# Optimization experiments

Measured on AMD Instinct MI355X. Metric: run time of the kernel, lower is better.

## Reference

```python
import jax, jax.numpy as jnp
import numpy as np

N = 50000      # nodes
E = 800000     # edges (before self-loops)
IN = 256       # input_dim
H = 8          # heads (hard-coded in module)
C = 32         # hidden_dim per head
OUT = 64       # output_dim
NEG_SLOPE = 0.2  # PyG GATConv default leaky_relu slope


def setup_inputs() -> dict:
    key = jax.random.key(0)
    ks = jax.random.split(key, 8)
    x = jax.random.normal(ks[0], (N, IN), dtype=jnp.float32)
    edge_index = jax.random.randint(ks[1], (2, E), 0, N, dtype=jnp.int64)
    # GATConv params (concat=True -> out width H*C)
    W_gat = jax.random.normal(ks[2], (IN, H * C), dtype=jnp.float32) * (1.0 / np.sqrt(IN))
    att_src = jax.random.normal(ks[3], (1, H, C), dtype=jnp.float32) * (1.0 / np.sqrt(C))
    att_dst = jax.random.normal(ks[4], (1, H, C), dtype=jnp.float32) * (1.0 / np.sqrt(C))
    bias_gat = jnp.zeros((H * C,), dtype=jnp.float32)
    # final Linear
    W_lin = jax.random.normal(ks[5], (H * C, OUT), dtype=jnp.float32) * (1.0 / np.sqrt(H * C))
    b_lin = jnp.zeros((OUT,), dtype=jnp.float32)
    return {"x": x, "edge_index": edge_index, "W_gat": W_gat, "att_src": att_src,
            "att_dst": att_dst, "bias_gat": bias_gat, "W_lin": W_lin, "b_lin": b_lin}


def reference(x, edge_index, W_gat, att_src, att_dst, bias_gat, W_lin, b_lin):
    # add self-loops (PyG GATConv default add_self_loops=True)
    ar = jnp.arange(N, dtype=edge_index.dtype)
    ei = jnp.concatenate([edge_index, jnp.stack([ar, ar])], axis=1)  # [2, E+N]
    src, dst = ei[0], ei[1]

    h = (x @ W_gat).reshape(N, H, C)                # [N,H,C]
    a_src = jnp.sum(h * att_src, axis=-1)           # [N,H]
    a_dst = jnp.sum(h * att_dst, axis=-1)           # [N,H]

    e = a_src[src] + a_dst[dst]                     # [E+N,H] per-edge logits
    e = jnp.where(e > 0, e, NEG_SLOPE * e)          # leaky_relu

    # segment softmax over incoming edges of each dst node
    m = jax.ops.segment_max(e, dst, num_segments=N)           # [N,H]
    ex = jnp.exp(e - m[dst])                                   # [E+N,H]
    denom = jax.ops.segment_sum(ex, dst, num_segments=N)       # [N,H]
    alpha = ex / (denom[dst] + 1e-16)                           # [E+N,H]

    msg = h[src] * alpha[:, :, None]                            # [E+N,H,C]
    out = jax.ops.segment_sum(msg, dst, num_segments=N)        # [N,H,C]
    out = out.reshape(N, H * C) + bias_gat                      # concat heads + bias

    out = jax.nn.relu(out)
    return out @ W_lin + b_lin                                  # [N,OUT]
```

## Files before the change

### kernel.cpp

```cpp
#include <hip/hip_runtime.h>
#include <hip/hip_bf16.h>

typedef __attribute__((ext_vector_type(8))) short short8v;
typedef __attribute__((ext_vector_type(4))) float floatx4;

__device__ __forceinline__ unsigned short f2bf(float f) {
    unsigned b = __float_as_uint(f);
    b = (b + 0x7fffu + ((b >> 16) & 1u)) >> 16;
    return (unsigned short)b;
}
__device__ __forceinline__ float b2f(unsigned short u) {
    return __uint_as_float((unsigned)u << 16);
}

__global__ void k_prep(const float* __restrict__ x, unsigned short* __restrict__ xb, int n0,
                       const float* __restrict__ Wg, unsigned short* __restrict__ wbT,
                       const float* __restrict__ Wl, unsigned short* __restrict__ wlbT,
                       const int* __restrict__ ei, int* __restrict__ cnt, int E) {
    const int TG = 256 * 256 / 4;
    const int TL = 256 * 64 / 4;
    int total = n0 + TG + TL + E;
    int i = blockIdx.x * blockDim.x + threadIdx.x;
    int stride = gridDim.x * blockDim.x;
    for (; i < total; i += stride) {
        if (i < n0) {
            float4 v = reinterpret_cast<const float4*>(x)[i];
            ushort4 o;
            o.x = f2bf(v.x); o.y = f2bf(v.y); o.z = f2bf(v.z); o.w = f2bf(v.w);
            reinterpret_cast<ushort4*>(xb)[i] = o;
        } else if (i < n0 + TG) {
            int j = i - n0;
            int k = j >> 6, c4 = (j & 63) * 4;
            float4 v = *reinterpret_cast<const float4*>(Wg + k * 256 + c4);
            wbT[(size_t)(c4 + 0) * 256 + k] = f2bf(v.x);
            wbT[(size_t)(c4 + 1) * 256 + k] = f2bf(v.y);
            wbT[(size_t)(c4 + 2) * 256 + k] = f2bf(v.z);
            wbT[(size_t)(c4 + 3) * 256 + k] = f2bf(v.w);
        } else if (i < n0 + TG + TL) {
            int j = i - n0 - TG;
            int k = j >> 4, c4 = (j & 15) * 4;
            float4 v = *reinterpret_cast<const float4*>(Wl + k * 64 + c4);
            wlbT[(size_t)(c4 + 0) * 256 + k] = f2bf(v.x);
            wlbT[(size_t)(c4 + 1) * 256 + k] = f2bf(v.y);
            wlbT[(size_t)(c4 + 2) * 256 + k] = f2bf(v.z);
            wlbT[(size_t)(c4 + 3) * 256 + k] = f2bf(v.w);
        } else {
            int e = i - n0 - TG - TL;
            atomicAdd(&cnt[ei[E + e]], 1);
        }
    }
}

#define SCAN_NB 256
__launch_bounds__(256)
__global__ void k_scan_a(const int* __restrict__ cnt, int* __restrict__ bsum, int N) {
    __shared__ int sh[256];
    int b = blockIdx.x, t = threadIdx.x;
    int chunk = (N + SCAN_NB - 1) / SCAN_NB;
    int idx = b * chunk + t;
    sh[t] = (t < chunk && idx < N) ? (cnt[idx] + 1) : 0;
    __syncthreads();
    for (int off = 128; off > 0; off >>= 1) {
        if (t < off) sh[t] += sh[t + off];
        __syncthreads();
    }
    if (t == 0) bsum[b] = sh[0];
}
__launch_bounds__(256)
__global__ void k_scan_bc(const int* __restrict__ cnt, const int* __restrict__ bsum,
                          int* __restrict__ row_start, int* __restrict__ cursor,
                          unsigned short* __restrict__ ssrc, int N) {
    __shared__ int shb[256];
    __shared__ int sh[256];
    int b = blockIdx.x, t = threadIdx.x;
    shb[t] = bsum[t];
    __syncthreads();
    for (int off = 1; off < 256; off <<= 1) {
        int v = (t >= off) ? shb[t - off] : 0;
        __syncthreads();
        shb[t] += v;
        __syncthreads();
    }
    int boff = (b == 0) ? 0 : shb[b - 1];

    int chunk = (N + SCAN_NB - 1) / SCAN_NB;
    int idx = b * chunk + t;
    int v = (t < chunk && idx < N) ? (cnt[idx] + 1) : 0;
    sh[t] = v;
    __syncthreads();
    for (int off = 1; off < 256; off <<= 1) {
        int u = (t >= off) ? sh[t - off] : 0;
        __syncthreads();
        sh[t] += u;
        __syncthreads();
    }
    if (t < chunk && idx < N) {
        int ex = boff + sh[t] - v;
        row_start[idx] = ex;
        cursor[idx] = ex + 1;
        ssrc[ex] = (unsigned short)idx;
    }
}

__launch_bounds__(512)
__global__ void k_gs(const unsigned short* __restrict__ A,
                     const unsigned short* __restrict__ BT,
                     const float* __restrict__ att_src, const float* __restrict__ att_dst,
                     unsigned short* __restrict__ hb,
                     float* __restrict__ a_src, float* __restrict__ a_dst,
                     int M, int RB, int GB1,
                     const int* __restrict__ ei, int* __restrict__ cursor,
                     unsigned short* __restrict__ ssrc, int E) {
    __shared__ unsigned short BsT[64 * 264];
    const int b = blockIdx.x;
    const int tid = threadIdx.x;
    if (b >= GB1) {
        int e0 = ((b - GB1) * 512 + tid) * 4;
        if (e0 >= E) return;
        int4 s4 = *reinterpret_cast<const int4*>(ei + e0);
        int4 d4 = *reinterpret_cast<const int4*>(ei + E + e0);
        int p0 = atomicAdd(&cursor[d4.x], 1);
        int p1 = atomicAdd(&cursor[d4.y], 1);
        int p2 = atomicAdd(&cursor[d4.z], 1);
        int p3 = atomicAdd(&cursor[d4.w], 1);
        ssrc[p0] = (unsigned short)s4.x;
        ssrc[p1] = (unsigned short)s4.y;
        ssrc[p2] = (unsigned short)s4.z;
        ssrc[p3] = (unsigned short)s4.w;
        return;
    }
    const int nt = b / RB;
    const int tM = (b - nt * RB) * 128;

#pragma unroll
    for (int it = 0; it < 4; ++it) {
        int chunk = it * 512 + tid;
        int col = chunk >> 5;
        int k0 = (chunk & 31) * 8;
        short8v v = *reinterpret_cast<const short8v*>(BT + (size_t)(nt * 64 + col) * 256 + k0);
        *reinterpret_cast<short8v*>(&BsT[col * 264 + k0]) = v;
    }
    __syncthreads();

    const int w  = tid >> 6;
    const int l  = tid & 63;
    const int lg = l >> 4;
    const int lr = l & 15;

    int rowA = tM + w * 16 + lr;
    if (rowA > M - 1) rowA = M - 1;
    const unsigned short* Arow = A + (size_t)rowA * 256 + lg * 8;
    short8v av[8];
#pragma unroll
    for (int kt = 0; kt < 8; ++kt)
        av[kt] = *reinterpret_cast<const short8v*>(Arow + kt * 32);

    floatx4 acc[4] = {};
#pragma unroll
    for (int kt = 0; kt < 8; ++kt) {
#pragma unroll
        for (int n = 0; n < 4; ++n) {
            short8v bv = *reinterpret_cast<const short8v*>(&BsT[(n * 16 + lr) * 264 + kt * 32 + lg * 8]);
            acc[n] = __builtin_amdgcn_mfma_f32_16x16x32_bf16(av[kt], bv, acc[n], 0, 0, 0);
        }
    }

    float ps[2][4] = {}, pd[2][4] = {};
#pragma unroll
    for (int n = 0; n < 4; ++n) {
        int hd2 = n >> 1;
        float asv = att_src[(nt * 2 + hd2) * 32 + (n & 1) * 16 + lr];
        float adv = att_dst[(nt * 2 + hd2) * 32 + (n & 1) * 16 + lr];
        int col = nt * 64 + n * 16 + lr;
#pragma unroll
        for (int r = 0; r < 4; ++r) {
            int row = tM + w * 16 + lg * 4 + r;
            float v = acc[n][r];
            if (row < M) hb[(size_t)row * 256 + col] = f2bf(v);
            ps[hd2][r] += v * asv;
            pd[hd2][r] += v * adv;
        }
    }
#pragma unroll
    for (int off = 1; off < 16; off <<= 1) {
#pragma unroll
        for (int hd2 = 0; hd2 < 2; ++hd2)
#pragma unroll
            for (int r = 0; r < 4; ++r) {
                ps[hd2][r] += __shfl_xor(ps[hd2][r], off, 64);
                pd[hd2][r] += __shfl_xor(pd[hd2][r], off, 64);
            }
    }
    if (lr == 0) {
#pragma unroll
        for (int hd2 = 0; hd2 < 2; ++hd2)
#pragma unroll
            for (int r = 0; r < 4; ++r) {
                int row = tM + w * 16 + lg * 4 + r;
                if (row < M) {
                    a_src[(size_t)row * 8 + nt * 2 + hd2] = ps[hd2][r];
                    a_dst[(size_t)row * 8 + nt * 2 + hd2] = pd[hd2][r];
                }
            }
    }
}

__launch_bounds__(512)
__global__ void k_gemm2(const unsigned short* __restrict__ A,
                        const unsigned short* __restrict__ BT,
                        float* __restrict__ C,
                        const float* __restrict__ bias, int M) {
    __shared__ unsigned short BsT[64 * 264];
    const int tid = threadIdx.x;
    const int tM = blockIdx.x * 128;

#pragma unroll
    for (int it = 0; it < 4; ++it) {
        int chunk = it * 512 + tid;
        int col = chunk >> 5;
        int k0 = (chunk & 31) * 8;
        short8v v = *reinterpret_cast<const short8v*>(BT + (size_t)col * 256 + k0);
        *reinterpret_cast<short8v*>(&BsT[col * 264 + k0]) = v;
    }
    __syncthreads();

    const int w  = tid >> 6;
    const int l  = tid & 63;
    const int lg = l >> 4;
    const int lr = l & 15;

    int rowA = tM + w * 16 + lr;
    if (rowA > M - 1) rowA = M - 1;
    const unsigned short* Arow = A + (size_t)rowA * 256 + lg * 8;

    floatx4 acc[4] = {};
#pragma unroll
    for (int kt = 0; kt < 8; ++kt) {
        short8v av = *reinterpret_cast<const short8v*>(Arow + kt * 32);
#pragma unroll
        for (int n = 0; n < 4; ++n) {
            short8v bv = *reinterpret_cast<const short8v*>(&BsT[(n * 16 + lr) * 264 + kt * 32 + lg * 8]);
            acc[n] = __builtin_amdgcn_mfma_f32_16x16x32_bf16(av, bv, acc[n], 0, 0, 0);
        }
    }
#pragma unroll
    for (int n = 0; n < 4; ++n) {
        int col = n * 16 + lr;
        float badd = bias[col];
#pragma unroll
        for (int r = 0; r < 4; ++r) {
            int row = tM + w * 16 + lg * 4 + r;
            if (row < M) C[(size_t)row * 64 + col] = acc[n][r] + badd;
        }
    }
}

__launch_bounds__(256)
__global__ void k_agg(const int* __restrict__ row_start, const int* __restrict__ row_end,
                      const unsigned short* __restrict__ sorted_src,
                      const float* __restrict__ a_src, const float* __restrict__ a_dst,
                      const unsigned short* __restrict__ hb,
                      const float* __restrict__ bias_gat,
                      unsigned short* __restrict__ gb, int N) {
    int n = blockIdx.x * 4 + (threadIdx.x >> 6);
    if (n >= N) return;
    int lane = threadIdx.x & 63;
    int hd = lane >> 3;
    int start = row_start[n], end = row_end[n];
    float ad = a_dst[(size_t)n * 8 + hd];
    float ax = 0.f, ay = 0.f, az = 0.f, aw = 0.f, den = 0.f;
    float bx = 0.f, by = 0.f, bz = 0.f, bw = 0.f, den2 = 0.f;
    for (int j0 = start; j0 < end; j0 += 64) {
        int idx = j0 + lane;
        int sv = (idx < end) ? (int)sorted_src[idx] : 0;
        int cnt = end - j0; if (cnt > 64) cnt = 64;
        int jj = 0;
        for (; jj + 3 < cnt; jj += 4) {
            int s0 = __shfl(sv, jj);
            int s1 = __shfl(sv, jj + 1);
            int s2 = __shfl(sv, jj + 2);
            int s3 = __shfl(sv, jj + 3);
            float v0 = a_src[(size_t)s0 * 8 + hd] + ad;
            float v1 = a_src[(size_t)s1 * 8 + hd] + ad;
            float v2 = a_src[(size_t)s2 * 8 + hd] + ad;
            float v3 = a_src[(size_t)s3 * 8 + hd] + ad;
            ushort4 h0 = *reinterpret_cast<const ushort4*>(hb + (size_t)s0 * 256 + lane * 4);
            ushort4 h1 = *reinterpret_cast<const ushort4*>(hb + (size_t)s1 * 256 + lane * 4);
            ushort4 h2 = *reinterpret_cast<const ushort4*>(hb + (size_t)s2 * 256 + lane * 4);
            ushort4 h3 = *reinterpret_cast<const ushort4*>(hb + (size_t)s3 * 256 + lane * 4);
            v0 = v0 > 0.f ? v0 : 0.2f * v0;
            v1 = v1 > 0.f ? v1 : 0.2f * v1;
            v2 = v2 > 0.f ? v2 : 0.2f * v2;
            v3 = v3 > 0.f ? v3 : 0.2f * v3;
            float e0 = __expf(v0), e1 = __expf(v1), e2 = __expf(v2), e3 = __expf(v3);
            den  += e0 + e2; den2 += e1 + e3;
            ax += e0 * b2f(h0.x); ay += e0 * b2f(h0.y);
            az += e0 * b2f(h0.z); aw += e0 * b2f(h0.w);
            bx += e1 * b2f(h1.x); by += e1 * b2f(h1.y);
            bz += e1 * b2f(h1.z); bw += e1 * b2f(h1.w);
            ax += e2 * b2f(h2.x); ay += e2 * b2f(h2.y);
            az += e2 * b2f(h2.z); aw += e2 * b2f(h2.w);
            bx += e3 * b2f(h3.x); by += e3 * b2f(h3.y);
            bz += e3 * b2f(h3.z); bw += e3 * b2f(h3.w);
        }
        for (; jj < cnt; ++jj) {
            int s0 = __shfl(sv, jj);
            float v0 = a_src[(size_t)s0 * 8 + hd] + ad;
            v0 = v0 > 0.f ? v0 : 0.2f * v0;
            float e0 = __expf(v0);
            ushort4 h0 = *reinterpret_cast<const ushort4*>(hb + (size_t)s0 * 256 + lane * 4);
            den += e0;
            ax += e0 * b2f(h0.x); ay += e0 * b2f(h0.y);
            az += e0 * b2f(h0.z); aw += e0 * b2f(h0.w);
        }
    }
    float inv = 1.0f / (den + den2 + 1e-16f);
    float4 b4 = *reinterpret_cast<const float4*>(bias_gat + lane * 4);
    ushort4 o;
    o.x = f2bf(fmaxf((ax + bx) * inv + b4.x, 0.f));
    o.y = f2bf(fmaxf((ay + by) * inv + b4.y, 0.f));
    o.z = f2bf(fmaxf((az + bz) * inv + b4.z, 0.f));
    o.w = f2bf(fmaxf((aw + bw) * inv + b4.w, 0.f));
    reinterpret_cast<ushort4*>(gb)[(size_t)n * 64 + lane] = o;
}

extern "C" void kernel_launch(void* const* d_in, const int* in_sizes, int n_in,
                              void* d_out, int out_size, void* d_ws, size_t ws_size,
                              hipStream_t stream) {
    const float* x        = (const float*)d_in[0];
    const int*   ei       = (const int*)d_in[1];
    const float* W_gat    = (const float*)d_in[2];
    const float* att_src  = (const float*)d_in[3];
    const float* att_dst  = (const float*)d_in[4];
    const float* bias_gat = (const float*)d_in[5];
    const float* W_lin    = (const float*)d_in[6];
    const float* b_lin    = (const float*)d_in[7];
    float* out = (float*)d_out;

    const int N  = in_sizes[0] / 256;
    const int E  = in_sizes[1] / 2;
    const int EE = E + N;

    char* ws = (char*)d_ws;
    size_t off = 0;
    auto alloc = [&](size_t bytes) -> void* {
        void* p = ws + off;
        off = (off + bytes + 255) & ~(size_t)255;
        return p;
    };
    unsigned short* hb       = (unsigned short*)alloc((size_t)N * 256 * 2);
    float*          a_srcv   = (float*)alloc((size_t)N * 8 * 4);
    float*          a_dstv   = (float*)alloc((size_t)N * 8 * 4);
    int*            cnt      = (int*)alloc((size_t)N * 4);
    int*            rowst    = (int*)alloc((size_t)N * 4);
    int*            cursor   = (int*)alloc((size_t)N * 4);
    int*            bsum     = (int*)alloc(SCAN_NB * 4);
    unsigned short* ssrc     = (unsigned short*)alloc((size_t)EE * 2);
    unsigned short* xb       = (unsigned short*)alloc((size_t)N * 256 * 2);
    unsigned short* wbT      = (unsigned short*)alloc(256 * 256 * 2);
    unsigned short* wlbT     = (unsigned short*)alloc(64 * 256 * 2);

    hipMemsetAsync(cnt, 0, (size_t)N * 4, stream);

    k_prep<<<2048, 256, 0, stream>>>(x, xb, N * 256 / 4,
                                     W_gat, wbT, W_lin, wlbT, ei, cnt, E);

    k_scan_a<<<SCAN_NB, 256, 0, stream>>>(cnt, bsum, N);
    k_scan_bc<<<SCAN_NB, 256, 0, stream>>>(cnt, bsum, rowst, cursor, ssrc, N);

    const int RB  = (N + 127) / 128;
    const int GB1 = RB * 4;
    const int SB  = (E / 4 + 511) / 512;
    k_gs<<<GB1 + SB, 512, 0, stream>>>(xb, wbT, att_src, att_dst, hb, a_srcv, a_dstv,
                                       N, RB, GB1, ei, cursor, ssrc, E);

    k_agg<<<(N + 3) / 4, 256, 0, stream>>>(rowst, cursor, ssrc, a_srcv, a_dstv, hb,
                                           bias_gat, xb, N);

    k_gemm2<<<(N + 127) / 128, 512, 0, stream>>>(xb, wlbT, out, b_lin, N);
}
```

Measured before the change: 195.2 us.

## Split prep into histogram kernel, overlap conversions with scans, widen aggregation loads

Replaces the monolithic prep kernel with a dedicated vectorized histogram kernel and moves the x/W bf16 conversions into extra blocks of the two scan kernels, so the conversion work runs alongside the small scan grids. It also rewrites the aggregation kernel so each half-wave handles a different edge using 16-byte loads of 8 features per lane, then combines the halves with cross-lane shuffles. This aims to hide the latency of the tiny scan launches and to halve the number of gather instructions per edge. The cost is extra shuffle reductions and lanes that sit idle during the final store.

```diff
diff --git a/kernel.cpp b/kernel.cpp
--- a/kernel.cpp
+++ b/kernel.cpp
@@ -13,49 +13,50 @@
     return __uint_as_float((unsigned)u << 16);
 }
 
-__global__ void k_prep(const float* __restrict__ x, unsigned short* __restrict__ xb, int n0,
-                       const float* __restrict__ Wg, unsigned short* __restrict__ wbT,
-                       const float* __restrict__ Wl, unsigned short* __restrict__ wlbT,
-                       const int* __restrict__ ei, int* __restrict__ cnt, int E) {
-    const int TG = 256 * 256 / 4;
-    const int TL = 256 * 64 / 4;
-    int total = n0 + TG + TL + E;
-    int i = blockIdx.x * blockDim.x + threadIdx.x;
-    int stride = gridDim.x * blockDim.x;
-    for (; i < total; i += stride) {
-        if (i < n0) {
-            float4 v = reinterpret_cast<const float4*>(x)[i];
-            ushort4 o;
-            o.x = f2bf(v.x); o.y = f2bf(v.y); o.z = f2bf(v.z); o.w = f2bf(v.w);
-            reinterpret_cast<ushort4*>(xb)[i] = o;
-        } else if (i < n0 + TG) {
-            int j = i - n0;
-            int k = j >> 6, c4 = (j & 63) * 4;
-            float4 v = *reinterpret_cast<const float4*>(Wg + k * 256 + c4);
-            wbT[(size_t)(c4 + 0) * 256 + k] = f2bf(v.x);
-            wbT[(size_t)(c4 + 1) * 256 + k] = f2bf(v.y);
-            wbT[(size_t)(c4 + 2) * 256 + k] = f2bf(v.z);
-            wbT[(size_t)(c4 + 3) * 256 + k] = f2bf(v.w);
-        } else if (i < n0 + TG + TL) {
-            int j = i - n0 - TG;
-            int k = j >> 4, c4 = (j & 15) * 4;
-            float4 v = *reinterpret_cast<const float4*>(Wl + k * 64 + c4);
-            wlbT[(size_t)(c4 + 0) * 256 + k] = f2bf(v.x);
-            wlbT[(size_t)(c4 + 1) * 256 + k] = f2bf(v.y);
-            wlbT[(size_t)(c4 + 2) * 256 + k] = f2bf(v.z);
-            wlbT[(size_t)(c4 + 3) * 256 + k] = f2bf(v.w);
-        } else {
-            int e = i - n0 - TG - TL;
-            atomicAdd(&cnt[ei[E + e]], 1);
-        }
-    }
-}
-
 #define SCAN_NB 256
+
+__device__ __forceinline__ void conv_x(const float* __restrict__ x,
+                                       unsigned short* __restrict__ xb, int i) {
+    float4 v = reinterpret_cast<const float4*>(x)[i];
+    ushort4 o;
+    o.x = f2bf(v.x); o.y = f2bf(v.y); o.z = f2bf(v.z); o.w = f2bf(v.w);
+    reinterpret_cast<ushort4*>(xb)[i] = o;
+}
+__device__ __forceinline__ void conv_wT(const float* __restrict__ W,
+                                        unsigned short* __restrict__ wT,
+                                        int j, int NC) {
+    int k = j / (NC / 4), c4 = (j % (NC / 4)) * 4;
+    float4 v = *reinterpret_cast<const float4*>(W + (size_t)k * NC + c4);
+    wT[(size_t)(c4 + 0) * 256 + k] = f2bf(v.x);
+    wT[(size_t)(c4 + 1) * 256 + k] = f2bf(v.y);
+    wT[(size_t)(c4 + 2) * 256 + k] = f2bf(v.z);
+    wT[(size_t)(c4 + 3) * 256 + k] = f2bf(v.w);
+}
+
+__global__ void k_hist(const int* __restrict__ ei, int* __restrict__ cnt, int E) {
+    int e0 = (blockIdx.x * 256 + threadIdx.x) * 4;
+    if (e0 >= E) return;
+    int4 d4 = *reinterpret_cast<const int4*>(ei + E + e0);
+    atomicAdd(&cnt[d4.x], 1);
+    atomicAdd(&cnt[d4.y], 1);
+    atomicAdd(&cnt[d4.z], 1);
+    atomicAdd(&cnt[d4.w], 1);
+}
+
 __launch_bounds__(256)
-__global__ void k_scan_a(const int* __restrict__ cnt, int* __restrict__ bsum, int N) {
+__global__ void k_scan_a(const int* __restrict__ cnt, int* __restrict__ bsum, int N,
+                         const float* __restrict__ x, unsigned short* __restrict__ xb,
+                         int xh1,
+                         const float* __restrict__ Wg, unsigned short* __restrict__ wbT,
+                         int TG) {
+    int b = blockIdx.x, t = threadIdx.x;
+    if (b >= SCAN_NB) {
+        int i = (b - SCAN_NB) * 256 + t;
+        if (i < xh1) conv_x(x, xb, i);
+        else if (i < xh1 + TG) conv_wT(Wg, wbT, i - xh1, 256);
+        return;
+    }
     __shared__ int sh[256];
-    int b = blockIdx.x, t = threadIdx.x;
     int chunk = (N + SCAN_NB - 1) / SCAN_NB;
     int idx = b * chunk + t;
     sh[t] = (t < chunk && idx < N) ? (cnt[idx] + 1) : 0;
@@ -66,13 +67,24 @@
     }
     if (t == 0) bsum[b] = sh[0];
 }
+
 __launch_bounds__(256)
 __global__ void k_scan_bc(const int* __restrict__ cnt, const int* __restrict__ bsum,
                           int* __restrict__ row_start, int* __restrict__ cursor,
-                          unsigned short* __restrict__ ssrc, int N) {
+                          unsigned short* __restrict__ ssrc, int N,
+                          const float* __restrict__ x, unsigned short* __restrict__ xb,
+                          int xh1, int xh2,
+                          const float* __restrict__ Wl, unsigned short* __restrict__ wlbT,
+                          int TL) {
+    int b = blockIdx.x, t = threadIdx.x;
+    if (b >= SCAN_NB) {
+        int i = (b - SCAN_NB) * 256 + t;
+        if (i < xh2) conv_x(x, xb, xh1 + i);
+        else if (i < xh2 + TL) conv_wT(Wl, wlbT, i - xh2, 64);
+        return;
+    }
     __shared__ int shb[256];
     __shared__ int sh[256];
-    int b = blockIdx.x, t = threadIdx.x;
     shb[t] = bsum[t];
     __syncthreads();
     for (int off = 1; off < 256; off <<= 1) {
@@ -264,64 +276,64 @@
                       unsigned short* __restrict__ gb, int N) {
     int n = blockIdx.x * 4 + (threadIdx.x >> 6);
     if (n >= N) return;
-    int lane = threadIdx.x & 63;
-    int hd = lane >> 3;
+    const int lane = threadIdx.x & 63;
+    const int half = lane >> 5;
+    const int li   = lane & 31;
+    const int hd   = li >> 2;
     int start = row_start[n], end = row_end[n];
     float ad = a_dst[(size_t)n * 8 + hd];
-    float ax = 0.f, ay = 0.f, az = 0.f, aw = 0.f, den = 0.f;
-    float bx = 0.f, by = 0.f, bz = 0.f, bw = 0.f, den2 = 0.f;
+    float accA[8] = {}, accB[8] = {};
+    float denA = 0.f, denB = 0.f;
     for (int j0 = start; j0 < end; j0 += 64) {
         int idx = j0 + lane;
         int sv = (idx < end) ? (int)sorted_src[idx] : 0;
         int cnt = end - j0; if (cnt > 64) cnt = 64;
         int jj = 0;
         for (; jj + 3 < cnt; jj += 4) {
-            int s0 = __shfl(sv, jj);
-            int s1 = __shfl(sv, jj + 1);
-            int s2 = __shfl(sv, jj + 2);
-            int s3 = __shfl(sv, jj + 3);
-            float v0 = a_src[(size_t)s0 * 8 + hd] + ad;
-            float v1 = a_src[(size_t)s1 * 8 + hd] + ad;
-            float v2 = a_src[(size_t)s2 * 8 + hd] + ad;
-            float v3 = a_src[(size_t)s3 * 8 + hd] + ad;
-            ushort4 h0 = *reinterpret_cast<const ushort4*>(hb + (size_t)s0 * 256 + lane * 4);
-            ushort4 h1 = *reinterpret_cast<const ushort4*>(hb + (size_t)s1 * 256 + lane * 4);
-            ushort4 h2 = *reinterpret_cast<const ushort4*>(hb + (size_t)s2 * 256 + lane * 4);
-            ushort4 h3 = *reinterpret_cast<const ushort4*>(hb + (size_t)s3 * 256 + lane * 4);
-            v0 = v0 > 0.f ? v0 : 0.2f * v0;
-            v1 = v1 > 0.f ? v1 : 0.2f * v1;
-            v2 = v2 > 0.f ? v2 : 0.2f * v2;
-            v3 = v3 > 0.f ? v3 : 0.2f * v3;
-            float e0 = __expf(v0), e1 = __expf(v1), e2 = __expf(v2), e3 = __expf(v3);
-            den  += e0 + e2; den2 += e1 + e3;
-            ax += e0 * b2f(h0.x); ay += e0 * b2f(h0.y);
-            az += e0 * b2f(h0.z); aw += e0 * b2f(h0.w);
-            bx += e1 * b2f(h1.x); by += e1 * b2f(h1.y);
-            bz += e1 * b2f(h1.z); bw += e1 * b2f(h1.w);
-            ax += e2 * b2f(h2.x); ay += e2 * b2f(h2.y);
-            az += e2 * b2f(h2.z); aw += e2 * b2f(h2.w);
-            bx += e3 * b2f(h3.x); by += e3 * b2f(h3.y);
-            bz += e3 * b2f(h3.z); bw += e3 * b2f(h3.w);
-        }
-        for (; jj < cnt; ++jj) {
-            int s0 = __shfl(sv, jj);
-            float v0 = a_src[(size_t)s0 * 8 + hd] + ad;
-            v0 = v0 > 0.f ? v0 : 0.2f * v0;
-            float e0 = __expf(v0);
-            ushort4 h0 = *reinterpret_cast<const ushort4*>(hb + (size_t)s0 * 256 + lane * 4);
-            den += e0;
-            ax += e0 * b2f(h0.x); ay += e0 * b2f(h0.y);
-            az += e0 * b2f(h0.z); aw += e0 * b2f(h0.w);
-        }
-    }
-    float inv = 1.0f / (den + den2 + 1e-16f);
-    float4 b4 = *reinterpret_cast<const float4*>(bias_gat + lane * 4);
-    ushort4 o;
-    o.x = f2bf(fmaxf((ax + bx) * inv + b4.x, 0.f));
-    o.y = f2bf(fmaxf((ay + by) * inv + b4.y, 0.f));
-    o.z = f2bf(fmaxf((az + bz) * inv + b4.z, 0.f));
-    o.w = f2bf(fmaxf((aw + bw) * inv + b4.w, 0.f));
-    reinterpret_cast<ushort4*>(gb)[(size_t)n * 64 + lane] = o;
+            int sA = __shfl(sv, jj + half);
+            int sB = __shfl(sv, jj + 2 + half);
+            float vA = a_src[(size_t)sA * 8 + hd] + ad;
+            float vB = a_src[(size_t)sB * 8 + hd] + ad;
+            short8v hA = *reinterpret_cast<const short8v*>(hb + (size_t)sA * 256 + li * 8);
+            short8v hB = *reinterpret_cast<const short8v*>(hb + (size_t)sB * 256 + li * 8);
+            vA = vA > 0.f ? vA : 0.2f * vA;
+            vB = vB > 0.f ? vB : 0.2f * vB;
+            float eA = __expf(vA), eB = __expf(vB);
+            denA += eA; denB += eB;
+#pragma unroll
+            for (int q = 0; q < 8; ++q) {
+                accA[q] += eA * b2f((unsigned short)hA[q]);
+                accB[q] += eB * b2f((unsigned short)hB[q]);
+            }
+        }
+        for (; jj < cnt; jj += 2) {
+            int jp = jj + half;
+            int s = __shfl(sv, (jp < cnt) ? jp : 0);
+            float v = a_src[(size_t)s * 8 + hd] + ad;
+            v = v > 0.f ? v : 0.2f * v;
+            float e = (jp < cnt) ? __expf(v) : 0.f;
+            short8v h8 = *reinterpret_cast<const short8v*>(hb + (size_t)s * 256 + li * 8);
+            denA += e;
+#pragma unroll
+            for (int q = 0; q < 8; ++q)
+                accA[q] += e * b2f((unsigned short)h8[q]);
+        }
+    }
+    float den = denA + denB;
+    den += __shfl_xor(den, 32, 64);
+    float inv = 1.0f / (den + 1e-16f);
+    float4 b0 = reinterpret_cast<const float4*>(bias_gat + li * 8)[0];
+    float4 b1 = reinterpret_cast<const float4*>(bias_gat + li * 8)[1];
+    float bb[8] = {b0.x, b0.y, b0.z, b0.w, b1.x, b1.y, b1.z, b1.w};
+    short8v o;
+#pragma unroll
+    for (int q = 0; q < 8; ++q) {
+        float s = accA[q] + accB[q];
+        s += __shfl_xor(s, 32, 64);
+        o[q] = (short)f2bf(fmaxf(s * inv + bb[q], 0.f));
+    }
+    if (half == 0)
+        *reinterpret_cast<short8v*>(gb + (size_t)n * 256 + li * 8) = o;
 }
 
 extern "C" void kernel_launch(void* const* d_in, const int* in_sizes, int n_in,
@@ -360,13 +372,22 @@
     unsigned short* wbT      = (unsigned short*)alloc(256 * 256 * 2);
     unsigned short* wlbT     = (unsigned short*)alloc(64 * 256 * 2);
 
+    const int n0  = N * 256 / 4;
+    const int xh1 = n0 / 2;
+    const int xh2 = n0 - xh1;
+    const int TG  = 256 * 256 / 4;
+    const int TL  = 256 * 64 / 4;
+
     hipMemsetAsync(cnt, 0, (size_t)N * 4, stream);
 
-    k_prep<<<2048, 256, 0, stream>>>(x, xb, N * 256 / 4,
-                                     W_gat, wbT, W_lin, wlbT, ei, cnt, E);
-
-    k_scan_a<<<SCAN_NB, 256, 0, stream>>>(cnt, bsum, N);
-    k_scan_bc<<<SCAN_NB, 256, 0, stream>>>(cnt, bsum, rowst, cursor, ssrc, N);
+    k_hist<<<(E / 4 + 255) / 256, 256, 0, stream>>>(ei, cnt, E);
+
+    int cb1 = (xh1 + TG + 255) / 256;
+    k_scan_a<<<SCAN_NB + cb1, 256, 0, stream>>>(cnt, bsum, N, x, xb, xh1, W_gat, wbT, TG);
+
+    int cb2 = (xh2 + TL + 255) / 256;
+    k_scan_bc<<<SCAN_NB + cb2, 256, 0, stream>>>(cnt, bsum, rowst, cursor, ssrc, N,
+                                                 x, xb, xh1, xh2, W_lin, wlbT, TL);
 
     const int RB  = (N + 127) / 128;
     const int GB1 = RB * 4;
```

Result: slower. 204.2 us (+4.7%).

## Fuse final linear layer into GAT aggregation kernel via per-block MFMA

Applied to the files above, without the earlier changes.

Removes the separate k_gemm2 launch. Each 4-node aggregation block now stages its bf16 ReLU outputs in shared memory and multiplies them by W_lin with a 16x16x32 MFMA per wave, writing the final fp32 output directly. This avoids writing the intermediate bf16 activations to global memory and reading them back. In exchange, every block re-reads the full 32KB W_lin from cache. Only 4 of the 16 MFMA rows carry valid data, and a block barrier now makes the waves of a block wait for the slowest node.

```diff
diff --git a/kernel.cpp b/kernel.cpp
--- a/kernel.cpp
+++ b/kernel.cpp
@@ -205,123 +205,99 @@
     }
 }
 
-__launch_bounds__(512)
-__global__ void k_gemm2(const unsigned short* __restrict__ A,
-                        const unsigned short* __restrict__ BT,
-                        float* __restrict__ C,
-                        const float* __restrict__ bias, int M) {
-    __shared__ unsigned short BsT[64 * 264];
-    const int tid = threadIdx.x;
-    const int tM = blockIdx.x * 128;
-
-#pragma unroll
-    for (int it = 0; it < 4; ++it) {
-        int chunk = it * 512 + tid;
-        int col = chunk >> 5;
-        int k0 = (chunk & 31) * 8;
-        short8v v = *reinterpret_cast<const short8v*>(BT + (size_t)col * 256 + k0);
-        *reinterpret_cast<short8v*>(&BsT[col * 264 + k0]) = v;
-    }
-    __syncthreads();
-
-    const int w  = tid >> 6;
-    const int l  = tid & 63;
-    const int lg = l >> 4;
-    const int lr = l & 15;
-
-    int rowA = tM + w * 16 + lr;
-    if (rowA > M - 1) rowA = M - 1;
-    const unsigned short* Arow = A + (size_t)rowA * 256 + lg * 8;
-
-    floatx4 acc[4] = {};
-#pragma unroll
-    for (int kt = 0; kt < 8; ++kt) {
-        short8v av = *reinterpret_cast<const short8v*>(Arow + kt * 32);
-#pragma unroll
-        for (int n = 0; n < 4; ++n) {
-            short8v bv = *reinterpret_cast<const short8v*>(&BsT[(n * 16 + lr) * 264 + kt * 32 + lg * 8]);
-            acc[n] = __builtin_amdgcn_mfma_f32_16x16x32_bf16(av, bv, acc[n], 0, 0, 0);
-        }
-    }
-#pragma unroll
-    for (int n = 0; n < 4; ++n) {
-        int col = n * 16 + lr;
-        float badd = bias[col];
-#pragma unroll
-        for (int r = 0; r < 4; ++r) {
-            int row = tM + w * 16 + lg * 4 + r;
-            if (row < M) C[(size_t)row * 64 + col] = acc[n][r] + badd;
-        }
-    }
-}
-
 __launch_bounds__(256)
 __global__ void k_agg(const int* __restrict__ row_start, const int* __restrict__ row_end,
                       const unsigned short* __restrict__ sorted_src,
                       const float* __restrict__ a_src, const float* __restrict__ a_dst,
                       const unsigned short* __restrict__ hb,
                       const float* __restrict__ bias_gat,
-                      unsigned short* __restrict__ gb, int N) {
-    int n = blockIdx.x * 4 + (threadIdx.x >> 6);
-    if (n >= N) return;
-    int lane = threadIdx.x & 63;
-    int hd = lane >> 3;
-    int start = row_start[n], end = row_end[n];
-    float ad = a_dst[(size_t)n * 8 + hd];
-    float ax = 0.f, ay = 0.f, az = 0.f, aw = 0.f, den = 0.f;
-    float bx = 0.f, by = 0.f, bz = 0.f, bw = 0.f, den2 = 0.f;
-    for (int j0 = start; j0 < end; j0 += 64) {
-        int idx = j0 + lane;
-        int sv = (idx < end) ? (int)sorted_src[idx] : 0;
-        int cnt = end - j0; if (cnt > 64) cnt = 64;
-        int jj = 0;
-        for (; jj + 3 < cnt; jj += 4) {
-            int s0 = __shfl(sv, jj);
-            int s1 = __shfl(sv, jj + 1);
-            int s2 = __shfl(sv, jj + 2);
-            int s3 = __shfl(sv, jj + 3);
-            float v0 = a_src[(size_t)s0 * 8 + hd] + ad;
-            float v1 = a_src[(size_t)s1 * 8 + hd] + ad;
-            float v2 = a_src[(size_t)s2 * 8 + hd] + ad;
-            float v3 = a_src[(size_t)s3 * 8 + hd] + ad;
-            ushort4 h0 = *reinterpret_cast<const ushort4*>(hb + (size_t)s0 * 256 + lane * 4);
-            ushort4 h1 = *reinterpret_cast<const ushort4*>(hb + (size_t)s1 * 256 + lane * 4);
-            ushort4 h2 = *reinterpret_cast<const ushort4*>(hb + (size_t)s2 * 256 + lane * 4);
-            ushort4 h3 = *reinterpret_cast<const ushort4*>(hb + (size_t)s3 * 256 + lane * 4);
-            v0 = v0 > 0.f ? v0 : 0.2f * v0;
-            v1 = v1 > 0.f ? v1 : 0.2f * v1;
-            v2 = v2 > 0.f ? v2 : 0.2f * v2;
-            v3 = v3 > 0.f ? v3 : 0.2f * v3;
-            float e0 = __expf(v0), e1 = __expf(v1), e2 = __expf(v2), e3 = __expf(v3);
-            den  += e0 + e2; den2 += e1 + e3;
-            ax += e0 * b2f(h0.x); ay += e0 * b2f(h0.y);
-            az += e0 * b2f(h0.z); aw += e0 * b2f(h0.w);
-            bx += e1 * b2f(h1.x); by += e1 * b2f(h1.y);
-            bz += e1 * b2f(h1.z); bw += e1 * b2f(h1.w);
-            ax += e2 * b2f(h2.x); ay += e2 * b2f(h2.y);
-            az += e2 * b2f(h2.z); aw += e2 * b2f(h2.w);
-            bx += e3 * b2f(h3.x); by += e3 * b2f(h3.y);
-            bz += e3 * b2f(h3.z); bw += e3 * b2f(h3.w);
-        }
-        for (; jj < cnt; ++jj) {
-            int s0 = __shfl(sv, jj);
-            float v0 = a_src[(size_t)s0 * 8 + hd] + ad;
-            v0 = v0 > 0.f ? v0 : 0.2f * v0;
-            float e0 = __expf(v0);
-            ushort4 h0 = *reinterpret_cast<const ushort4*>(hb + (size_t)s0 * 256 + lane * 4);
-            den += e0;
-            ax += e0 * b2f(h0.x); ay += e0 * b2f(h0.y);
-            az += e0 * b2f(h0.z); aw += e0 * b2f(h0.w);
-        }
-    }
-    float inv = 1.0f / (den + den2 + 1e-16f);
-    float4 b4 = *reinterpret_cast<const float4*>(bias_gat + lane * 4);
-    ushort4 o;
-    o.x = f2bf(fmaxf((ax + bx) * inv + b4.x, 0.f));
-    o.y = f2bf(fmaxf((ay + by) * inv + b4.y, 0.f));
-    o.z = f2bf(fmaxf((az + bz) * inv + b4.z, 0.f));
-    o.w = f2bf(fmaxf((aw + bw) * inv + b4.w, 0.f));
-    reinterpret_cast<ushort4*>(gb)[(size_t)n * 64 + lane] = o;
+                      const unsigned short* __restrict__ BT,
+                      const float* __restrict__ b_lin,
+                      float* __restrict__ out, int N) {
+    __shared__ unsigned short gsh[16 * 264];
+    const int w = threadIdx.x >> 6;
+    const int lane = threadIdx.x & 63;
+    int n = blockIdx.x * 4 + w;
+    if (n < N) {
+        int hd = lane >> 3;
+        int start = row_start[n], end = row_end[n];
+        float ad = a_dst[(size_t)n * 8 + hd];
+        float ax = 0.f, ay = 0.f, az = 0.f, aw = 0.f, den = 0.f;
+        float bx = 0.f, by = 0.f, bz = 0.f, bw = 0.f, den2 = 0.f;
+        for (int j0 = start; j0 < end; j0 += 64) {
+            int idx = j0 + lane;
+            int sv = (idx < end) ? (int)sorted_src[idx] : 0;
+            int cnt = end - j0; if (cnt > 64) cnt = 64;
+            int jj = 0;
+            for (; jj + 3 < cnt; jj += 4) {
+                int s0 = __shfl(sv, jj);
+                int s1 = __shfl(sv, jj + 1);
+                int s2 = __shfl(sv, jj + 2);
+                int s3 = __shfl(sv, jj + 3);
+                float v0 = a_src[(size_t)s0 * 8 + hd] + ad;
+                float v1 = a_src[(size_t)s1 * 8 + hd] + ad;
+                float v2 = a_src[(size_t)s2 * 8 + hd] + ad;
+                float v3 = a_src[(size_t)s3 * 8 + hd] + ad;
+                ushort4 h0 = *reinterpret_cast<const ushort4*>(hb + (size_t)s0 * 256 + lane * 4);
+                ushort4 h1 = *reinterpret_cast<const ushort4*>(hb + (size_t)s1 * 256 + lane * 4);
+                ushort4 h2 = *reinterpret_cast<const ushort4*>(hb + (size_t)s2 * 256 + lane * 4);
+                ushort4 h3 = *reinterpret_cast<const ushort4*>(hb + (size_t)s3 * 256 + lane * 4);
+                v0 = v0 > 0.f ? v0 : 0.2f * v0;
+                v1 = v1 > 0.f ? v1 : 0.2f * v1;
+                v2 = v2 > 0.f ? v2 : 0.2f * v2;
+                v3 = v3 > 0.f ? v3 : 0.2f * v3;
+                float e0 = __expf(v0), e1 = __expf(v1), e2 = __expf(v2), e3 = __expf(v3);
+                den  += e0 + e2; den2 += e1 + e3;
+                ax += e0 * b2f(h0.x); ay += e0 * b2f(h0.y);
+                az += e0 * b2f(h0.z); aw += e0 * b2f(h0.w);
+                bx += e1 * b2f(h1.x); by += e1 * b2f(h1.y);
+                bz += e1 * b2f(h1.z); bw += e1 * b2f(h1.w);
+                ax += e2 * b2f(h2.x); ay += e2 * b2f(h2.y);
+                az += e2 * b2f(h2.z); aw += e2 * b2f(h2.w);
+                bx += e3 * b2f(h3.x); by += e3 * b2f(h3.y);
+                bz += e3 * b2f(h3.z); bw += e3 * b2f(h3.w);
+            }
+            for (; jj < cnt; ++jj) {
+                int s0 = __shfl(sv, jj);
+                float v0 = a_src[(size_t)s0 * 8 + hd] + ad;
+                v0 = v0 > 0.f ? v0 : 0.2f * v0;
+                float e0 = __expf(v0);
+                ushort4 h0 = *reinterpret_cast<const ushort4*>(hb + (size_t)s0 * 256 + lane * 4);
+                den += e0;
+                ax += e0 * b2f(h0.x); ay += e0 * b2f(h0.y);
+                az += e0 * b2f(h0.z); aw += e0 * b2f(h0.w);
+            }
+        }
+        float inv = 1.0f / (den + den2 + 1e-16f);
+        float4 b4 = *reinterpret_cast<const float4*>(bias_gat + lane * 4);
+        ushort4 o;
+        o.x = f2bf(fmaxf((ax + bx) * inv + b4.x, 0.f));
+        o.y = f2bf(fmaxf((ay + by) * inv + b4.y, 0.f));
+        o.z = f2bf(fmaxf((az + bz) * inv + b4.z, 0.f));
+        o.w = f2bf(fmaxf((aw + bw) * inv + b4.w, 0.f));
+        *reinterpret_cast<ushort4*>(&gsh[w * 264 + lane * 4]) = o;
+    }
+    __syncthreads();
+
+    const int lg = lane >> 4;
+    const int lr = lane & 15;
+    const unsigned short* Bt = BT + (size_t)(w * 16 + lr) * 256 + lg * 8;
+    floatx4 acc = {};
+#pragma unroll
+    for (int kt = 0; kt < 8; ++kt) {
+        short8v av = *reinterpret_cast<const short8v*>(&gsh[lr * 264 + kt * 32 + lg * 8]);
+        short8v bv = *reinterpret_cast<const short8v*>(Bt + kt * 32);
+        acc = __builtin_amdgcn_mfma_f32_16x16x32_bf16(av, bv, acc, 0, 0, 0);
+    }
+    if (lg == 0) {
+        int col = w * 16 + lr;
+        float badd = b_lin[col];
+#pragma unroll
+        for (int r = 0; r < 4; ++r) {
+            int row = blockIdx.x * 4 + r;
+            if (row < N) out[(size_t)row * 64 + col] = acc[r] + badd;
+        }
+    }
 }
 
 extern "C" void kernel_launch(void* const* d_in, const int* in_sizes, int n_in,
@@ -375,7 +351,5 @@
                                        N, RB, GB1, ei, cursor, ssrc, E);
 
     k_agg<<<(N + 3) / 4, 256, 0, stream>>>(rowst, cursor, ssrc, a_srcv, a_dstv, hb,
-                                           bias_gat, xb, N);
-
-    k_gemm2<<<(N + 127) / 128, 512, 0, stream>>>(xb, wlbT, out, b_lin, N);
-}
+                                           bias_gat, wlbT, b_lin, out, N);
+}
```

Result: slower. 214.3 us (+9.8%).
